# Optimization experiments

Hardware: AMD Instinct MI355X
Metric: run time of the kernel (lower is better)

Reference implementation:

```python
import jax, jax.numpy as jnp
import numpy as np

B, H, I = 4096, 256, 32


def setup_inputs() -> dict:
    key = jax.random.key(0)
    k1, k2, k3, k4, k5 = jax.random.split(key, 5)
    idx = jax.random.randint(k1, (B,), 0, I)
    inp = jax.nn.one_hot(idx, I, dtype=jnp.float32)  # one-hot selector [B, I]
    hx = jax.random.normal(k2, (B, H), jnp.float32)
    weight_hh = jax.random.normal(k3, (3 * H, H, I), jnp.float32)
    bias_ih = jax.random.normal(k4, (3 * H, I), jnp.float32)
    bias_hh = jax.random.normal(k5, (3 * H, I), jnp.float32)
    return {"input": inp, "hx": hx, "weight_hh": weight_hh,
            "bias_ih": bias_ih, "bias_hh": bias_hh}


def reference(input, hx, weight_hh, bias_ih, bias_hh):
    # input is one-hot, so the broadcast-multiply-sum over the last axis is
    # mathematically a gather of the selected expert slice.
    idx = jnp.argmax(input, axis=-1)                      # [B]
    Wt = jnp.moveaxis(weight_hh, 2, 0)[idx]               # [B, 3H, H] selected recurrent weights
    rec = jnp.einsum('bgh,bh->bg', Wt, hx)                # [B, 3H]
    gates_i = bias_ih.T[idx]                              # [B, 3H]
    gates_h = rec + bias_hh.T[idx]                        # [B, 3H]
    ri, ui, ni = jnp.split(gates_i, 3, axis=1)
    rh, uh, nh = jnp.split(gates_h, 3, axis=1)
    reset_gate = jax.nn.sigmoid(ri + rh)
    update_gate = jax.nn.sigmoid(ui + uh)
    new_gate = jnp.tanh(ni + reset_gate * nh)
    hy = update_gate * hx + (1 - update_gate) * new_gate  # [B, H]
    return hy[None]
```

## Files before the change

kernel.cpp:

```cpp
#include <hip/hip_runtime.h>
#include <math.h>

#define B_N 4096
#define H_N 256
#define I_N 32
#define G3  768
#define NSEG 16
#define BKROW 4096

#define WS_SC      0
#define WS_BUCKET  2048
#define WS_B4      526336
#define WS_W5      657408
#define WS_NEEDED  13240320

typedef __attribute__((ext_vector_type(8))) _Float16 f16x8_t;
typedef __attribute__((ext_vector_type(4))) float f32x4_t;

__device__ __forceinline__ float sigm(float x) { return 1.0f / (1.0f + __expf(-x)); }
__device__ __forceinline__ float tanh_fast(float x) {
    float xc = fminf(fmaxf(x, -15.f), 15.f);
    float t = __expf(2.f * xc);
    return (t - 1.f) / (t + 1.f);
}

__global__ __launch_bounds__(256) void k_aux(
    const float* __restrict__ w, unsigned short* __restrict__ w5,
    const float* __restrict__ b_ih, const float* __restrict__ b_hh,
    float4* __restrict__ b4,
    const float* __restrict__ inp, int* __restrict__ sc,
    int* __restrict__ bucket)
{
    int bid = blockIdx.x;
    int t = threadIdx.x;
    if (bid < 768) {
        __shared__ float tl[8 * 1057];
        int r0 = (bid >> 3) * 8;
        int ks = bid & 7;
#pragma unroll
        for (int it = 0; it < 8; ++it) {
            int f4 = it * 256 + t;
            int e4 = (f4 & 7) * 4, hh = (f4 >> 3) & 31, r = f4 >> 8;
            float4 v = *(const float4*)(w + ((size_t)(r0 + r) * 256 + ks * 32 + hh) * 32 + e4);
            int bse = r * 1057 + hh * 33 + e4;
            tl[bse] = v.x; tl[bse + 1] = v.y; tl[bse + 2] = v.z; tl[bse + 3] = v.w;
        }
        __syncthreads();
        int rowgrp = r0 >> 4;
        int mbase = r0 & 15;
#pragma unroll
        for (int it = 0; it < 4; ++it) {
            int c = it * 256 + t;
            int m8 = c & 7, kg = (c >> 3) & 3, e = c >> 5;
            union { _Float16 h[8]; uint4 v; } hi;
#pragma unroll
            for (int t8 = 0; t8 < 8; ++t8) {
                float f = tl[m8 * 1057 + (kg * 8 + t8) * 33 + e];
                hi.h[t8] = (_Float16)f;
            }
            size_t chunk = ((size_t)(e * 8 + ks) * 48 + rowgrp) * 64 + kg * 16 + mbase + m8;
            ((uint4*)w5)[chunk] = hi.v;
        }
    } else if (bid < 800) {
        int bb = bid - 768;
        int e = t & 31;
        int tt = bb * 8 + (t >> 5);
        float r = b_ih[tt * 32 + e] + b_hh[tt * 32 + e];
        float u = b_ih[(256 + tt) * 32 + e] + b_hh[(256 + tt) * 32 + e];
        float ni = b_ih[(512 + tt) * 32 + e];
        float nh = b_hh[(512 + tt) * 32 + e];
        float4 o = {r, u, ni, nh};
        b4[e * 256 + tt] = o;
    } else {
        __shared__ int lhist[32];
        int seg = bid - 800;
        if (t < 32) lhist[t] = 0;
        __syncthreads();
        int b = seg * 256 + t;
        const float4* p = (const float4*)(inp + (size_t)b * I_N);
        int idx = 0;
#pragma unroll
        for (int k = 0; k < 8; ++k) {
            float4 v = p[k];
            if (v.x > 0.5f) idx = k * 4 + 0;
            if (v.y > 0.5f) idx = k * 4 + 1;
            if (v.z > 0.5f) idx = k * 4 + 2;
            if (v.w > 0.5f) idx = k * 4 + 3;
        }
        int lp = atomicAdd(&lhist[idx], 1);
        bucket[idx * BKROW + seg * 256 + lp] = b;
        __syncthreads();
        if (t < 32) sc[seg * 32 + t] = lhist[t];
    }
}

__global__ __launch_bounds__(256, 4) void k_gemm_mfma(
    const unsigned short* __restrict__ w5,
    const float* __restrict__ hx, const float4* __restrict__ b4,
    const int* __restrict__ sc, const int* __restrict__ bucket,
    float* __restrict__ out)
{
    int bkt = blockIdx.x & 7, j0 = blockIdx.x >> 3;
    int t = threadIdx.x;

    int tot0 = 0, tot1 = 0, tot2 = 0, tot3 = 0;
#pragma unroll
    for (int j = 0; j < NSEG; ++j) {
        tot0 += sc[j * 32 + bkt];
        tot1 += sc[j * 32 + bkt + 8];
        tot2 += sc[j * 32 + bkt + 16];
        tot3 += sc[j * 32 + bkt + 24];
    }
    int c1 = (tot0 + 15) >> 4;
    int c2 = c1 + ((tot1 + 15) >> 4);
    int c3 = c2 + ((tot2 + 15) >> 4);
    int ntot = c3 + ((tot3 + 15) >> 4);

    __shared__ _Float16 Ah[16 * 256];
    __shared__ int bids[16];

    int lane = t & 63, wv = t >> 6;
    int m16 = lane & 15, kg = lane >> 4;
    int q = blockIdx.y * 4 + wv;

    for (int jj = j0; jj < ntot; jj += 34) {
        int ei = (jj < c1) ? 0 : (jj < c2) ? 1 : (jj < c3) ? 2 : 3;
        int ch = (jj < c1) ? jj : (jj < c2) ? jj - c1 : (jj < c3) ? jj - c2 : jj - c3;
        int te = (jj < c1) ? tot0 : (jj < c2) ? tot1 : (jj < c3) ? tot2 : tot3;
        int e = bkt + 8 * ei;
        int M = te - ch * 16; if (M > 16) M = 16;

        const unsigned short* b_p = w5 + ((size_t)(e * 8) * 48 + q) * 512 + (size_t)lane * 8;
        f16x8_t bc0 = *(const f16x8_t*)(b_p);
        f16x8_t bc1 = *(const f16x8_t*)(b_p + (size_t)16 * 512);
        f16x8_t bc2 = *(const f16x8_t*)(b_p + (size_t)32 * 512);

        int row = t >> 4, c16 = t & 15;
        int b = -1;
        if (row < M) {
            int rank = ch * 16 + row;
            int acc = 0, seg = 0, off = 0;
#pragma unroll
            for (int j = 0; j < NSEG; ++j) {
                int c = sc[j * 32 + e];
                if (rank >= acc && rank < acc + c) { seg = j; off = rank - acc; }
                acc += c;
            }
            b = bucket[e * BKROW + seg * 256 + off];
        }
        if (c16 == 0) bids[row] = b;

        if (b >= 0) {
            const float* src = hx + ((size_t)b << 8) + c16 * 16;
            float fv[16];
#pragma unroll
            for (int p = 0; p < 4; ++p)
                *(float4*)&fv[p * 4] = *(const float4*)(src + p * 4);
#pragma unroll
            for (int p = 0; p < 2; ++p) {
                union { _Float16 h[8]; uint4 v; } hu;
#pragma unroll
                for (int jj2 = 0; jj2 < 8; ++jj2)
                    hu.h[jj2] = (_Float16)fv[p * 8 + jj2];
                int col = (c16 * 2 + p) ^ (row & 7);
                *(uint4*)&Ah[row * 256 + col * 8] = hu.v;
            }
        } else {
            uint4 z = {0, 0, 0, 0};
#pragma unroll
            for (int p = 0; p < 2; ++p) {
                int col = (c16 * 2 + p) ^ (row & 7);
                *(uint4*)&Ah[row * 256 + col * 8] = z;
            }
        }
        __syncthreads();

        f32x4_t ac0 = {0.f, 0.f, 0.f, 0.f};
        f32x4_t ac1 = {0.f, 0.f, 0.f, 0.f};
        f32x4_t ac2 = {0.f, 0.f, 0.f, 0.f};

#pragma unroll
        for (int ks = 0; ks < 8; ++ks) {
            f16x8_t bn0 = bc0, bn1 = bc1, bn2 = bc2;
            if (ks < 7) {
                const unsigned short* np = b_p + (size_t)(ks + 1) * 48 * 512;
                bn0 = *(const f16x8_t*)(np);
                bn1 = *(const f16x8_t*)(np + (size_t)16 * 512);
                bn2 = *(const f16x8_t*)(np + (size_t)32 * 512);
            }
            int sw = ((ks * 4 + kg) ^ (m16 & 7)) << 3;
            f16x8_t a0 = *(const f16x8_t*)&Ah[m16 * 256 + sw];
            ac0 = __builtin_amdgcn_mfma_f32_16x16x32_f16(a0, bc0, ac0, 0, 0, 0);
            ac1 = __builtin_amdgcn_mfma_f32_16x16x32_f16(a0, bc1, ac1, 0, 0, 0);
            ac2 = __builtin_amdgcn_mfma_f32_16x16x32_f16(a0, bc2, ac2, 0, 0, 0);
            bc0 = bn0; bc1 = bn1; bc2 = bn2;
        }

        int mg = (lane >> 4) * 4;
        int tt = q * 16 + m16;
        float4 bs = b4[e * 256 + tt];
#pragma unroll
        for (int i = 0; i < 4; ++i) {
            int mr = mg + i;
            if (mr < M) {
                int bb = bids[mr];
                int xc = ((tt >> 3) ^ (mr & 7)) * 8 + (tt & 7);
                float x = (float)Ah[mr * 256 + xc];
                float r = sigm(ac0[i] + bs.x);
                float u = sigm(ac1[i] + bs.y);
                float n = tanh_fast(bs.z + r * (ac2[i] + bs.w));
                out[(size_t)bb * 256 + tt] = u * x + (1.0f - u) * n;
            }
        }
        __syncthreads();
    }
}

__global__ void k_naive(const float* __restrict__ inp, const float* __restrict__ hx,
                        const float* __restrict__ w, const float* __restrict__ b_ih,
                        const float* __restrict__ b_hh, float* __restrict__ out) {
    int b = blockIdx.x;
    int t = threadIdx.x;
    __shared__ float sx[H_N];
    __shared__ int sidx;
    if (t == 0) {
        int idx = 0;
        for (int i = 0; i < I_N; ++i)
            if (inp[b * I_N + i] > 0.5f) idx = i;
        sidx = idx;
    }
    sx[t] = hx[b * H_N + t];
    __syncthreads();
    int i = sidx;
    float a0 = 0.f, a1 = 0.f, a2 = 0.f;
    for (int h = 0; h < H_N; ++h) {
        float xv = sx[h];
        a0 = fmaf(w[(t * H_N + h) * I_N + i], xv, a0);
        a1 = fmaf(w[((256 + t) * H_N + h) * I_N + i], xv, a1);
        a2 = fmaf(w[((512 + t) * H_N + h) * I_N + i], xv, a2);
    }
    float r = sigm(b_ih[t * I_N + i] + a0 + b_hh[t * I_N + i]);
    float u = sigm(b_ih[(256 + t) * I_N + i] + a1 + b_hh[(256 + t) * I_N + i]);
    float n = tanhf(b_ih[(512 + t) * I_N + i] + r * (a2 + b_hh[(512 + t) * I_N + i]));
    out[b * H_N + t] = u * sx[t] + (1.0f - u) * n;
}

extern "C" void kernel_launch(void* const* d_in, const int* in_sizes, int n_in,
                              void* d_out, int out_size, void* d_ws, size_t ws_size,
                              hipStream_t stream) {
    const float* inp  = (const float*)d_in[0];
    const float* hx   = (const float*)d_in[1];
    const float* w    = (const float*)d_in[2];
    const float* b_ih = (const float*)d_in[3];
    const float* b_hh = (const float*)d_in[4];
    float* out = (float*)d_out;

    if (ws_size < (size_t)WS_NEEDED) {
        k_naive<<<B_N, H_N, 0, stream>>>(inp, hx, w, b_ih, b_hh, out);
        return;
    }

    char* ws = (char*)d_ws;
    int* sc     = (int*)(ws + WS_SC);
    int* bucket = (int*)(ws + WS_BUCKET);
    float4* b4  = (float4*)(ws + WS_B4);
    unsigned short* w5 = (unsigned short*)(ws + WS_W5);

    k_aux<<<816, 256, 0, stream>>>(w, w5, b_ih, b_hh, b4, inp, sc, bucket);
    k_gemm_mfma<<<dim3(272, 4), 256, 0, stream>>>(w5, hx, b4, sc, bucket, out);
}
```

Measured before the change: 27.16 us.

## Swap MFMA operands to load hx directly into registers, drop shared-memory staging

The grouped GEMM kernel now puts the weight fragment in the A operand and the hidden-state rows in the B operand, so each lane loads its own hx slice from global memory and converts it to fp16 in registers instead of staging a 16x256 tile in LDS. This removes the shared-memory tile, the bids array and both block barriers per chunk. The epilogue now reads x from fp32 hx and writes four contiguous outputs per lane as a float4. Each wave now redundantly loads and converts the hx rows, and the bucket index lookup is repeated per lane.

```diff
diff --git a/kernel.cpp b/kernel.cpp
--- a/kernel.cpp
+++ b/kernel.cpp
@@ -116,11 +116,8 @@
     int c3 = c2 + ((tot2 + 15) >> 4);
     int ntot = c3 + ((tot3 + 15) >> 4);
 
-    __shared__ _Float16 Ah[16 * 256];
-    __shared__ int bids[16];
-
     int lane = t & 63, wv = t >> 6;
-    int m16 = lane & 15, kg = lane >> 4;
+    int m = lane & 15, kg = lane >> 4;
     int q = blockIdx.y * 4 + wv;
 
     for (int jj = j0; jj < ntot; jj += 34) {
@@ -131,49 +128,29 @@
         int M = te - ch * 16; if (M > 16) M = 16;
 
         const unsigned short* b_p = w5 + ((size_t)(e * 8) * 48 + q) * 512 + (size_t)lane * 8;
-        f16x8_t bc0 = *(const f16x8_t*)(b_p);
-        f16x8_t bc1 = *(const f16x8_t*)(b_p + (size_t)16 * 512);
-        f16x8_t bc2 = *(const f16x8_t*)(b_p + (size_t)32 * 512);
-
-        int row = t >> 4, c16 = t & 15;
+        f16x8_t wc0 = *(const f16x8_t*)(b_p);
+        f16x8_t wc1 = *(const f16x8_t*)(b_p + (size_t)16 * 512);
+        f16x8_t wc2 = *(const f16x8_t*)(b_p + (size_t)32 * 512);
+
         int b = -1;
-        if (row < M) {
-            int rank = ch * 16 + row;
-            int acc = 0, seg = 0, off = 0;
-#pragma unroll
-            for (int j = 0; j < NSEG; ++j) {
-                int c = sc[j * 32 + e];
-                if (rank >= acc && rank < acc + c) { seg = j; off = rank - acc; }
-                acc += c;
-            }
-            b = bucket[e * BKROW + seg * 256 + off];
-        }
-        if (c16 == 0) bids[row] = b;
-
-        if (b >= 0) {
-            const float* src = hx + ((size_t)b << 8) + c16 * 16;
-            float fv[16];
-#pragma unroll
-            for (int p = 0; p < 4; ++p)
-                *(float4*)&fv[p * 4] = *(const float4*)(src + p * 4);
-#pragma unroll
-            for (int p = 0; p < 2; ++p) {
-                union { _Float16 h[8]; uint4 v; } hu;
-#pragma unroll
-                for (int jj2 = 0; jj2 < 8; ++jj2)
-                    hu.h[jj2] = (_Float16)fv[p * 8 + jj2];
-                int col = (c16 * 2 + p) ^ (row & 7);
-                *(uint4*)&Ah[row * 256 + col * 8] = hu.v;
-            }
-        } else {
-            uint4 z = {0, 0, 0, 0};
-#pragma unroll
-            for (int p = 0; p < 2; ++p) {
-                int col = (c16 * 2 + p) ^ (row & 7);
-                *(uint4*)&Ah[row * 256 + col * 8] = z;
-            }
-        }
-        __syncthreads();
+        {
+            int rank = ch * 16 + m;
+            if (m < M) {
+                int acc = 0, seg = 0, off = 0;
+#pragma unroll
+                for (int j = 0; j < NSEG; ++j) {
+                    int c = sc[j * 32 + e];
+                    if (rank >= acc && rank < acc + c) { seg = j; off = rank - acc; }
+                    acc += c;
+                }
+                b = bucket[e * BKROW + seg * 256 + off];
+            }
+        }
+        int bidc = (b >= 0) ? b : 0;
+        const float* xsrc = hx + ((size_t)bidc << 8) + kg * 8;
+
+        float4 xa = *(const float4*)(xsrc);
+        float4 xb = *(const float4*)(xsrc + 4);
 
         f32x4_t ac0 = {0.f, 0.f, 0.f, 0.f};
         f32x4_t ac1 = {0.f, 0.f, 0.f, 0.f};
@@ -181,38 +158,42 @@
 
 #pragma unroll
         for (int ks = 0; ks < 8; ++ks) {
-            f16x8_t bn0 = bc0, bn1 = bc1, bn2 = bc2;
+            f16x8_t wn0 = wc0, wn1 = wc1, wn2 = wc2;
+            float4 xna = xa, xnb = xb;
             if (ks < 7) {
                 const unsigned short* np = b_p + (size_t)(ks + 1) * 48 * 512;
-                bn0 = *(const f16x8_t*)(np);
-                bn1 = *(const f16x8_t*)(np + (size_t)16 * 512);
-                bn2 = *(const f16x8_t*)(np + (size_t)32 * 512);
-            }
-            int sw = ((ks * 4 + kg) ^ (m16 & 7)) << 3;
-            f16x8_t a0 = *(const f16x8_t*)&Ah[m16 * 256 + sw];
-            ac0 = __builtin_amdgcn_mfma_f32_16x16x32_f16(a0, bc0, ac0, 0, 0, 0);
-            ac1 = __builtin_amdgcn_mfma_f32_16x16x32_f16(a0, bc1, ac1, 0, 0, 0);
-            ac2 = __builtin_amdgcn_mfma_f32_16x16x32_f16(a0, bc2, ac2, 0, 0, 0);
-            bc0 = bn0; bc1 = bn1; bc2 = bn2;
-        }
-
-        int mg = (lane >> 4) * 4;
-        int tt = q * 16 + m16;
-        float4 bs = b4[e * 256 + tt];
-#pragma unroll
-        for (int i = 0; i < 4; ++i) {
-            int mr = mg + i;
-            if (mr < M) {
-                int bb = bids[mr];
-                int xc = ((tt >> 3) ^ (mr & 7)) * 8 + (tt & 7);
-                float x = (float)Ah[mr * 256 + xc];
+                wn0 = *(const f16x8_t*)(np);
+                wn1 = *(const f16x8_t*)(np + (size_t)16 * 512);
+                wn2 = *(const f16x8_t*)(np + (size_t)32 * 512);
+                xna = *(const float4*)(xsrc + (ks + 1) * 32);
+                xnb = *(const float4*)(xsrc + (ks + 1) * 32 + 4);
+            }
+            f16x8_t xf = { (_Float16)xa.x, (_Float16)xa.y, (_Float16)xa.z,
+                           (_Float16)xa.w, (_Float16)xb.x, (_Float16)xb.y,
+                           (_Float16)xb.z, (_Float16)xb.w };
+            ac0 = __builtin_amdgcn_mfma_f32_16x16x32_f16(wc0, xf, ac0, 0, 0, 0);
+            ac1 = __builtin_amdgcn_mfma_f32_16x16x32_f16(wc1, xf, ac1, 0, 0, 0);
+            ac2 = __builtin_amdgcn_mfma_f32_16x16x32_f16(wc2, xf, ac2, 0, 0, 0);
+            wc0 = wn0; wc1 = wn1; wc2 = wn2;
+            xa = xna; xb = xnb;
+        }
+
+        if (b >= 0) {
+            int u0 = q * 16 + kg * 4;
+            float4 xv = *(const float4*)(hx + ((size_t)b << 8) + u0);
+            float xr[4] = {xv.x, xv.y, xv.z, xv.w};
+            float orr[4];
+#pragma unroll
+            for (int i = 0; i < 4; ++i) {
+                float4 bs = b4[e * 256 + u0 + i];
                 float r = sigm(ac0[i] + bs.x);
                 float u = sigm(ac1[i] + bs.y);
                 float n = tanh_fast(bs.z + r * (ac2[i] + bs.w));
-                out[(size_t)bb * 256 + tt] = u * x + (1.0f - u) * n;
-            }
-        }
-        __syncthreads();
+                orr[i] = u * xr[i] + (1.0f - u) * n;
+            }
+            float4 ov = {orr[0], orr[1], orr[2], orr[3]};
+            *(float4*)(out + ((size_t)b << 8) + u0) = ov;
+        }
     }
 }
 
```

Result: slower. 33.96 us (+25.0%).
